# Kernel tuning notes

Hardware: AMD Instinct MI355X
Metric: run time of the kernel (lower is better)

## Reference

```python
import jax, jax.numpy as jnp
import numpy as np

N_NODES = 50000
N_EDGES = 800000
D = 128
N_GRAPHS = 64


def setup_inputs() -> dict:
    key = jax.random.key(0)
    ks = jax.random.split(key, 10)
    x = jax.random.normal(ks[0], (N_NODES, D), dtype=jnp.float32)
    edge_weight = jax.random.uniform(ks[1], (N_EDGES,), dtype=jnp.float32)
    W1 = jax.random.normal(ks[2], (D, D), dtype=jnp.float32) / np.sqrt(D)
    b1 = jax.random.normal(ks[3], (D,), dtype=jnp.float32) * 0.01
    W2 = jax.random.normal(ks[4], (D, D), dtype=jnp.float32) / np.sqrt(D)
    b2 = jax.random.normal(ks[5], (D,), dtype=jnp.float32) * 0.01
    Wh = jax.random.normal(ks[6], (D, 1), dtype=jnp.float32) / np.sqrt(D)
    bh = jax.random.normal(ks[7], (1,), dtype=jnp.float32) * 0.01
    edge_index = jax.random.randint(ks[8], (2, N_EDGES), 0, N_NODES, dtype=jnp.int64)
    batch = jnp.sort(jax.random.randint(ks[9], (N_NODES,), 0, N_GRAPHS, dtype=jnp.int64))
    return {"x": x, "edge_weight": edge_weight, "W1": W1, "b1": b1,
            "W2": W2, "b2": b2, "Wh": Wh, "bh": bh,
            "edge_index": edge_index, "batch": batch}


def reference(x, edge_weight, W1, b1, W2, b2, Wh, bh, edge_index, batch):
    N = x.shape[0]
    # --- GCN normalization with self-loops (computed once; shared by layers) ---
    row, col = edge_index[0], edge_index[1]
    loop = jnp.arange(N, dtype=edge_index.dtype)
    row2 = jnp.concatenate([row, loop])   # source nodes
    col2 = jnp.concatenate([col, loop])   # target nodes
    ew2 = jnp.concatenate([edge_weight, jnp.ones((N,), dtype=x.dtype)])
    deg = jax.ops.segment_sum(ew2, col2, num_segments=N)
    dinv = jnp.where(deg > 0, jax.lax.rsqrt(deg), 0.0)
    norm = dinv[row2] * ew2 * dinv[col2]  # [E+N]

    def gcn_conv(h, W, b):
        h = h @ W                                   # [N, D_out]
        msg = norm[:, None] * h[row2]               # gather + scale, [E+N, D_out]
        return jax.ops.segment_sum(msg, col2, num_segments=N) + b

    # dropout is identity in eval mode
    h = jax.nn.relu(gcn_conv(x, W1, b1))
    h = jax.nn.relu(gcn_conv(h, W2, b2))

    # --- global mean pool over graphs ---
    counts = jax.ops.segment_sum(jnp.ones((N,), dtype=h.dtype), batch, num_segments=N_GRAPHS)
    pooled = jax.ops.segment_sum(h, batch, num_segments=N_GRAPHS)
    pooled = pooled / jnp.maximum(counts, 1.0)[:, None]
    return pooled @ Wh + bh
```

## Files before the change

kernel.cpp:

```cpp
#include <hip/hip_runtime.h>
#include <hip/hip_bf16.h>
#include <hip/hip_fp16.h>
#include <hip/hip_fp8.h>

#define N_NODES  50000
#define N_EDGES  800000
#define D        128
#define N_GRAPHS 64
#define CAP      64
#define EW_SCALE 1048576.0f
#define NB_GEMM1 391
#define NB_FILL  3125
#define NB_AGG16 3125

typedef _Float16 half8 __attribute__((ext_vector_type(8)));
typedef float   float4v __attribute__((ext_vector_type(4)));
typedef float   f32x2   __attribute__((ext_vector_type(2)));

__device__ __forceinline__ float2 h2f(unsigned int u) {
    __half2 h = *reinterpret_cast<__half2*>(&u);
    return __half22float2(h);
}
__device__ __forceinline__ float hu2f(unsigned short u) {
    __half_raw hr; hr.x = u;
    return __half2float(__half(hr));
}
__device__ __forceinline__ float2 fp8x2_f32(unsigned short u) {
    f32x2 v = __builtin_amdgcn_cvt_pk_f32_fp8((int)u, false);
    return make_float2(v[0], v[1]);
}
__device__ __forceinline__ unsigned char f32_fp8(float f) {
    __hip_fp8_e4m3 q(f);
    return (unsigned char)q.__x;
}
__device__ __forceinline__ void unpack_pd(unsigned long long p, int& n, float& dv) {
    int c = (int)(p >> 40);
    n = c < CAP ? c : CAP;
    dv = rsqrtf(1.0f + (float)(p & 0xFFFFFFFFFFULL) * (1.0f / EW_SCALE));
}

__global__ __launch_bounds__(256) void fused_gemm1_fill(const float* __restrict__ X,
                                                        const float* __restrict__ W,
                                                        unsigned char* __restrict__ Y8,
                                                        const int* __restrict__ ei,
                                                        const float* __restrict__ ew,
                                                        unsigned long long* __restrict__ packed,
                                                        unsigned int* __restrict__ bucket) {
    __shared__ float XT[32 * 128];
    __shared__ float Ws[32 * 128];

    if (blockIdx.x >= NB_GEMM1) {
        int e = (blockIdx.x - NB_GEMM1) * 256 + threadIdx.x;
        if (e >= N_EDGES) return;
        int r = ei[e];
        int c = ei[N_EDGES + e];
        float w = ew[e];
        unsigned long long add = (1ULL << 40) | (unsigned long long)(unsigned)(w * EW_SCALE + 0.5f);
        unsigned long long old = atomicAdd(&packed[c], add);
        unsigned pos = (unsigned)(old >> 40);
        if (pos < CAP) {
            unsigned short wh = __half_as_ushort(__float2half_rn(w));
            bucket[(size_t)c * CAP + pos] = (unsigned)r | ((unsigned)wh << 16);
        }
        return;
    }

    const int tid  = threadIdx.x;
    const int row0 = blockIdx.x * 128;
    const int tr = tid >> 4, tc = tid & 15;
    float acc[8][8] = {};

    for (int kt = 0; kt < 4; kt++) {
        const int kbase = kt * 32;
        {
            const float4* src = (const float4*)(W + kbase * 128);
            float4* dst = (float4*)Ws;
            for (int i = tid; i < 1024; i += 256) dst[i] = src[i];
        }
        {
            int r  = tid >> 1;
            int rr = row0 + r; if (rr >= N_NODES) rr = N_NODES - 1;
            int k0 = (tid & 1) * 16;
            const float4* src = (const float4*)(X + (size_t)rr * 128 + kbase + k0);
#pragma unroll
            for (int i = 0; i < 4; i++) {
                float4 v = src[i];
                int k = k0 + i * 4;
                XT[(k + 0) * 128 + r] = v.x;
                XT[(k + 1) * 128 + r] = v.y;
                XT[(k + 2) * 128 + r] = v.z;
                XT[(k + 3) * 128 + r] = v.w;
            }
        }
        __syncthreads();
#pragma unroll 4
        for (int k = 0; k < 32; k++) {
            float xs[8], ws[8];
            *(float4*)&xs[0] = *(const float4*)(XT + k * 128 + tr * 8);
            *(float4*)&xs[4] = *(const float4*)(XT + k * 128 + tr * 8 + 4);
            *(float4*)&ws[0] = *(const float4*)(Ws + k * 128 + tc * 8);
            *(float4*)&ws[4] = *(const float4*)(Ws + k * 128 + tc * 8 + 4);
#pragma unroll
            for (int i = 0; i < 8; i++)
#pragma unroll
                for (int j = 0; j < 8; j++)
                    acc[i][j] += xs[i] * ws[j];
        }
        __syncthreads();
    }
#pragma unroll
    for (int i = 0; i < 8; i++) {
        int r = row0 + tr * 8 + i;
        if (r < N_NODES) {
            uint2 p;
            p.x = (unsigned)f32_fp8(acc[i][0]) | ((unsigned)f32_fp8(acc[i][1]) << 8)
                | ((unsigned)f32_fp8(acc[i][2]) << 16) | ((unsigned)f32_fp8(acc[i][3]) << 24);
            p.y = (unsigned)f32_fp8(acc[i][4]) | ((unsigned)f32_fp8(acc[i][5]) << 8)
                | ((unsigned)f32_fp8(acc[i][6]) << 16) | ((unsigned)f32_fp8(acc[i][7]) << 24);
            *(uint2*)(Y8 + (size_t)r * 128 + tc * 8) = p;
        }
    }
}

__global__ __launch_bounds__(512) void agg1_gemm2_kernel(const unsigned char* __restrict__ x8in,
                                                         const unsigned long long* __restrict__ packed,
                                                         const unsigned int* __restrict__ bucket,
                                                         const float* __restrict__ b1,
                                                         const float* __restrict__ W2,
                                                         unsigned char* __restrict__ x2) {
    __shared__ _Float16 sh1[16][136];
    const int wv   = threadIdx.x >> 6;
    const int lane = threadIdx.x & 63;
    const unsigned short* xs16 = (const unsigned short*)x8in;
    const int node0 = blockIdx.x * 16;

    float2 bb = ((const float2*)b1)[lane];

    const int nodeA = node0 + wv * 2;
    const int nodeB = nodeA + 1;
    int nA; float dvA; unpack_pd(packed[nodeA], nA, dvA);
    int nB; float dvB; unpack_pd(packed[nodeB], nB, dvB);

    unsigned pkA = 0u, pkB = 0u;
    if (lane < nA) {
        unsigned eh = bucket[(size_t)nodeA * CAP + lane];
        int src = eh & 0xFFFFu;
        int sn; float sdv; unpack_pd(packed[src], sn, sdv);
        float v = hu2f((unsigned short)(eh >> 16)) * sdv;
        pkA = (unsigned)src | ((unsigned)__half_as_ushort(__float2half_rn(v)) << 16);
    }
    if (lane < nB) {
        unsigned eh = bucket[(size_t)nodeB * CAP + lane];
        int src = eh & 0xFFFFu;
        int sn; float sdv; unpack_pd(packed[src], sn, sdv);
        float v = hu2f((unsigned short)(eh >> 16)) * sdv;
        pkB = (unsigned)src | ((unsigned)__half_as_ushort(__float2half_rn(v)) << 16);
    }
    int pkiA = (int)pkA, pkiB = (int)pkB;

    float2 xsA = fp8x2_f32(xs16[(size_t)nodeA * 64 + lane]);
    float2 xsB = fp8x2_f32(xs16[(size_t)nodeB * 64 + lane]);
    float aAx = dvA * xsA.x, aAy = dvA * xsA.y;
    float aBx = dvB * xsB.x, aBy = dvB * xsB.y;

    int nmax = nA > nB ? nA : nB;
    for (int i = 0; i < nmax; i += 4) {
        unsigned a0 = (unsigned)__shfl(pkiA, i);
        unsigned a1 = (unsigned)__shfl(pkiA, i + 1);
        unsigned a2 = (unsigned)__shfl(pkiA, i + 2);
        unsigned a3 = (unsigned)__shfl(pkiA, i + 3);
        unsigned b0 = (unsigned)__shfl(pkiB, i);
        unsigned b1u = (unsigned)__shfl(pkiB, i + 1);
        unsigned b2 = (unsigned)__shfl(pkiB, i + 2);
        unsigned b3 = (unsigned)__shfl(pkiB, i + 3);
        unsigned short mA0 = xs16[(size_t)(a0 & 0xFFFF) * 64 + lane];
        unsigned short mA1 = xs16[(size_t)(a1 & 0xFFFF) * 64 + lane];
        unsigned short mA2 = xs16[(size_t)(a2 & 0xFFFF) * 64 + lane];
        unsigned short mA3 = xs16[(size_t)(a3 & 0xFFFF) * 64 + lane];
        unsigned short mB0 = xs16[(size_t)(b0 & 0xFFFF) * 64 + lane];
        unsigned short mB1 = xs16[(size_t)(b1u & 0xFFFF) * 64 + lane];
        unsigned short mB2 = xs16[(size_t)(b2 & 0xFFFF) * 64 + lane];
        unsigned short mB3 = xs16[(size_t)(b3 & 0xFFFF) * 64 + lane];
        float2 fA0 = fp8x2_f32(mA0), fA1 = fp8x2_f32(mA1);
        float2 fA2 = fp8x2_f32(mA2), fA3 = fp8x2_f32(mA3);
        float2 fB0 = fp8x2_f32(mB0), fB1 = fp8x2_f32(mB1);
        float2 fB2 = fp8x2_f32(mB2), fB3 = fp8x2_f32(mB3);
        float vA0 = hu2f((unsigned short)(a0 >> 16));
        float vA1 = hu2f((unsigned short)(a1 >> 16));
        float vA2 = hu2f((unsigned short)(a2 >> 16));
        float vA3 = hu2f((unsigned short)(a3 >> 16));
        float vB0 = hu2f((unsigned short)(b0 >> 16));
        float vB1 = hu2f((unsigned short)(b1u >> 16));
        float vB2 = hu2f((unsigned short)(b2 >> 16));
        float vB3 = hu2f((unsigned short)(b3 >> 16));
        aAx += vA0*fA0.x + vA1*fA1.x + vA2*fA2.x + vA3*fA3.x;
        aAy += vA0*fA0.y + vA1*fA1.y + vA2*fA2.y + vA3*fA3.y;
        aBx += vB0*fB0.x + vB1*fB1.x + vB2*fB2.x + vB3*fB3.x;
        aBy += vB0*fB0.y + vB1*fB1.y + vB2*fB2.y + vB3*fB3.y;
    }

    float hAx = fmaxf(dvA * aAx + bb.x, 0.0f);
    float hAy = fmaxf(dvA * aAy + bb.y, 0.0f);
    float hBx = fmaxf(dvB * aBx + bb.x, 0.0f);
    float hBy = fmaxf(dvB * aBy + bb.y, 0.0f);
    sh1[wv * 2][lane * 2]         = (_Float16)hAx;
    sh1[wv * 2][lane * 2 + 1]     = (_Float16)hAy;
    sh1[wv * 2 + 1][lane * 2]     = (_Float16)hBx;
    sh1[wv * 2 + 1][lane * 2 + 1] = (_Float16)hBy;
    __syncthreads();

    const int quad = lane >> 4;
    const int l16  = lane & 15;
    float4v acc0 = {};
#pragma unroll
    for (int kc = 0; kc < 4; kc++) {
        const int k0 = kc * 32;
        half8 a = *(const half8*)(&sh1[l16][k0 + quad * 8]);
        const float* wp = W2 + (size_t)(k0 + quad * 8) * 128 + wv * 16 + l16;
        half8 b;
#pragma unroll
        for (int jj = 0; jj < 8; jj++) b[jj] = (_Float16)wp[jj * 128];
        acc0 = __builtin_amdgcn_mfma_f32_16x16x32_f16(a, b, acc0, 0, 0, 0);
    }
#pragma unroll
    for (int r = 0; r < 4; r++) {
        int row = node0 + quad * 4 + r;
        int rn; float s;
        unpack_pd(packed[row], rn, s);
        x2[(size_t)row * 128 + wv * 16 + l16] = f32_fp8(acc0[r] * s);
    }
}

__global__ __launch_bounds__(256) void agg_head_kernel(const unsigned char* __restrict__ x8,
                                                       const unsigned long long* __restrict__ packed,
                                                       const unsigned int* __restrict__ bucket,
                                                       const float* __restrict__ bias,
                                                       const float* __restrict__ Wh,
                                                       float* __restrict__ nodedot) {
    const int wv   = threadIdx.x >> 6;
    const int lane = threadIdx.x & 63;
    const unsigned short* xs16 = (const unsigned short*)x8;

    const int nodeA = blockIdx.x * 8 + wv * 2;
    const int nodeB = nodeA + 1;
    int nA; float dvA; unpack_pd(packed[nodeA], nA, dvA);
    int nB; float dvB; unpack_pd(packed[nodeB], nB, dvB);

    unsigned ehA = (lane < nA) ? bucket[(size_t)nodeA * CAP + lane] : 0u;
    unsigned ehB = (lane < nB) ? bucket[(size_t)nodeB * CAP + lane] : 0u;
    int eiA = (int)ehA, eiB = (int)ehB;

    float2 xsA = fp8x2_f32(xs16[(size_t)nodeA * 64 + lane]);
    float2 xsB = fp8x2_f32(xs16[(size_t)nodeB * 64 + lane]);
    float aAx = xsA.x, aAy = xsA.y;
    float aBx = xsB.x, aBy = xsB.y;

    int nmax = nA > nB ? nA : nB;
    for (int i = 0; i < nmax; i += 4) {
        unsigned a0 = (unsigned)__shfl(eiA, i);
        unsigned a1 = (unsigned)__shfl(eiA, i + 1);
        unsigned a2 = (unsigned)__shfl(eiA, i + 2);
        unsigned a3 = (unsigned)__shfl(eiA, i + 3);
        unsigned b0 = (unsigned)__shfl(eiB, i);
        unsigned b1u = (unsigned)__shfl(eiB, i + 1);
        unsigned b2 = (unsigned)__shfl(eiB, i + 2);
        unsigned b3 = (unsigned)__shfl(eiB, i + 3);
        unsigned short mA0 = xs16[(size_t)(a0 & 0xFFFF) * 64 + lane];
        unsigned short mA1 = xs16[(size_t)(a1 & 0xFFFF) * 64 + lane];
        unsigned short mA2 = xs16[(size_t)(a2 & 0xFFFF) * 64 + lane];
        unsigned short mA3 = xs16[(size_t)(a3 & 0xFFFF) * 64 + lane];
        unsigned short mB0 = xs16[(size_t)(b0 & 0xFFFF) * 64 + lane];
        unsigned short mB1 = xs16[(size_t)(b1u & 0xFFFF) * 64 + lane];
        unsigned short mB2 = xs16[(size_t)(b2 & 0xFFFF) * 64 + lane];
        unsigned short mB3 = xs16[(size_t)(b3 & 0xFFFF) * 64 + lane];
        float2 fA0 = fp8x2_f32(mA0), fA1 = fp8x2_f32(mA1);
        float2 fA2 = fp8x2_f32(mA2), fA3 = fp8x2_f32(mA3);
        float2 fB0 = fp8x2_f32(mB0), fB1 = fp8x2_f32(mB1);
        float2 fB2 = fp8x2_f32(mB2), fB3 = fp8x2_f32(mB3);
        float vA0 = hu2f((unsigned short)(a0 >> 16));
        float vA1 = hu2f((unsigned short)(a1 >> 16));
        float vA2 = hu2f((unsigned short)(a2 >> 16));
        float vA3 = hu2f((unsigned short)(a3 >> 16));
        float vB0 = hu2f((unsigned short)(b0 >> 16));
        float vB1 = hu2f((unsigned short)(b1u >> 16));
        float vB2 = hu2f((unsigned short)(b2 >> 16));
        float vB3 = hu2f((unsigned short)(b3 >> 16));
        aAx += vA0*fA0.x + vA1*fA1.x + vA2*fA2.x + vA3*fA3.x;
        aAy += vA0*fA0.y + vA1*fA1.y + vA2*fA2.y + vA3*fA3.y;
        aBx += vB0*fB0.x + vB1*fB1.x + vB2*fB2.x + vB3*fB3.x;
        aBy += vB0*fB0.y + vB1*fB1.y + vB2*fB2.y + vB3*fB3.y;
    }

    float2 b = ((const float2*)bias)[lane];
    float2 w = ((const float2*)Wh)[lane];
    float hAx = fmaxf(dvA * aAx + b.x, 0.0f);
    float hAy = fmaxf(dvA * aAy + b.y, 0.0f);
    float hBx = fmaxf(dvB * aBx + b.x, 0.0f);
    float hBy = fmaxf(dvB * aBy + b.y, 0.0f);
    float sA = hAx * w.x + hAy * w.y;
    float sB = hBx * w.x + hBy * w.y;
#pragma unroll
    for (int off = 32; off > 0; off >>= 1) {
        sA += __shfl_down(sA, off, 64);
        sB += __shfl_down(sB, off, 64);
    }
    if (lane == 0) {
        nodedot[nodeA] = sA;
        nodedot[nodeB] = sB;
    }
}

__global__ __launch_bounds__(256) void final2_kernel(const float* __restrict__ nodedot,
                                                     const int* __restrict__ batch,
                                                     const float* __restrict__ bh,
                                                     float* __restrict__ out) {
    __shared__ float red[256];
    int g = blockIdx.x;
    int lo = 0, hi = N_NODES;
    while (lo < hi) { int mid = (lo + hi) >> 1; if (batch[mid] < g) lo = mid + 1; else hi = mid; }
    int a = lo;
    hi = N_NODES;
    while (lo < hi) { int mid = (lo + hi) >> 1; if (batch[mid] < g + 1) lo = mid + 1; else hi = mid; }
    int b = lo;

    float s = 0.0f;
    for (int n = a + threadIdx.x; n < b; n += 256) s += nodedot[n];
    red[threadIdx.x] = s;
    __syncthreads();
#pragma unroll
    for (int off = 128; off > 0; off >>= 1) {
        if (threadIdx.x < off) red[threadIdx.x] += red[threadIdx.x + off];
        __syncthreads();
    }
    if (threadIdx.x == 0)
        out[g] = red[0] / fmaxf((float)(b - a), 1.0f) + bh[0];
}

extern "C" void kernel_launch(void* const* d_in, const int* in_sizes, int n_in,
                              void* d_out, int out_size, void* d_ws, size_t ws_size,
                              hipStream_t stream) {
    const float* x   = (const float*)d_in[0];
    const float* ew  = (const float*)d_in[1];
    const float* W1  = (const float*)d_in[2];
    const float* b1  = (const float*)d_in[3];
    const float* W2  = (const float*)d_in[4];
    const float* b2  = (const float*)d_in[5];
    const float* Wh  = (const float*)d_in[6];
    const float* bh  = (const float*)d_in[7];
    const int*   ei  = (const int*)d_in[8];
    const int*   bat = (const int*)d_in[9];
    float* out = (float*)d_out;

    char* ws = (char*)d_ws;
    unsigned char* bufA8 = (unsigned char*)ws;            ws += (size_t)N_NODES * D;
    unsigned char* bufB8 = (unsigned char*)ws;            ws += (size_t)N_NODES * D;
    ws += 128 - ((size_t)ws & 127);
    unsigned int* bucket = (unsigned int*)ws;             ws += (size_t)N_NODES * CAP * 4;
    unsigned long long* packed = (unsigned long long*)ws; ws += (size_t)N_NODES * 8;
    float*  nodedot = (float*)ws;                         ws += (size_t)N_NODES * 4;

    const int nb_agg8 = N_NODES / 8;

    hipMemsetAsync(packed, 0, (size_t)N_NODES * 8, stream);

    fused_gemm1_fill<<<NB_GEMM1 + NB_FILL, 256, 0, stream>>>(x, W1, bufA8, ei, ew, packed, bucket);

    agg1_gemm2_kernel<<<NB_AGG16, 512, 0, stream>>>(bufA8, packed, bucket, b1, W2, bufB8);

    agg_head_kernel<<<nb_agg8, 256, 0, stream>>>(bufB8, packed, bucket, b2, Wh, nodedot);

    final2_kernel<<<N_GRAPHS, 256, 0, stream>>>(nodedot, bat, bh, out);
}
```

Measured before the change: 205.4 us.

## Use fp16 MFMA for first GEMM and deepen gather unroll in aggregation

The first layer's X@W1 GEMM moves from a scalar FP32 outer-product loop to fp16 MFMA 16x16x32 instructions. X and a transposed W tile are staged in padded half-precision shared memory. Both aggregation kernels now gather eight neighbours per iteration instead of four, putting more loads in flight. The cost is fp16 rounding of inputs before the GEMM, byte-wise (uncoalesced-ish) fp8 output stores, and extra register pressure from the deeper unroll.

```diff
diff --git a/kernel.cpp b/kernel.cpp
--- a/kernel.cpp
+++ b/kernel.cpp
@@ -14,6 +14,7 @@
 #define NB_AGG16 3125
 
 typedef _Float16 half8 __attribute__((ext_vector_type(8)));
+typedef _Float16 half4 __attribute__((ext_vector_type(4)));
 typedef float   float4v __attribute__((ext_vector_type(4)));
 typedef float   f32x2   __attribute__((ext_vector_type(2)));
 
@@ -46,8 +47,8 @@
                                                         const float* __restrict__ ew,
                                                         unsigned long long* __restrict__ packed,
                                                         unsigned int* __restrict__ bucket) {
-    __shared__ float XT[32 * 128];
-    __shared__ float Ws[32 * 128];
+    __shared__ _Float16 Xs[128][72];
+    __shared__ _Float16 Wt[128][72];
 
     if (blockIdx.x >= NB_GEMM1) {
         int e = (blockIdx.x - NB_GEMM1) * 256 + threadIdx.x;
@@ -67,16 +68,15 @@
 
     const int tid  = threadIdx.x;
     const int row0 = blockIdx.x * 128;
-    const int tr = tid >> 4, tc = tid & 15;
-    float acc[8][8] = {};
+    const int wv   = tid >> 6;
+    const int lane = tid & 63;
+    const int quad = lane >> 4;
+    const int l16  = lane & 15;
+
+    float4v acc[8][2] = {};
 
     for (int kt = 0; kt < 4; kt++) {
         const int kbase = kt * 32;
-        {
-            const float4* src = (const float4*)(W + kbase * 128);
-            float4* dst = (float4*)Ws;
-            for (int i = tid; i < 1024; i += 256) dst[i] = src[i];
-        }
         {
             int r  = tid >> 1;
             int rr = row0 + r; if (rr >= N_NODES) rr = N_NODES - 1;
@@ -85,41 +85,47 @@
 #pragma unroll
             for (int i = 0; i < 4; i++) {
                 float4 v = src[i];
-                int k = k0 + i * 4;
-                XT[(k + 0) * 128 + r] = v.x;
-                XT[(k + 1) * 128 + r] = v.y;
-                XT[(k + 2) * 128 + r] = v.z;
-                XT[(k + 3) * 128 + r] = v.w;
+                half4 hv;
+                hv[0] = (_Float16)v.x; hv[1] = (_Float16)v.y;
+                hv[2] = (_Float16)v.z; hv[3] = (_Float16)v.w;
+                *(half4*)(&Xs[r][k0 + i * 4]) = hv;
             }
         }
+        {
+            int k  = tid >> 3;
+            int c0 = (tid & 7) * 16;
+            const float4* src = (const float4*)(W + (size_t)(kbase + k) * 128 + c0);
+#pragma unroll
+            for (int i = 0; i < 4; i++) {
+                float4 v = src[i];
+                Wt[c0 + i * 4 + 0][k] = (_Float16)v.x;
+                Wt[c0 + i * 4 + 1][k] = (_Float16)v.y;
+                Wt[c0 + i * 4 + 2][k] = (_Float16)v.z;
+                Wt[c0 + i * 4 + 3][k] = (_Float16)v.w;
+            }
+        }
         __syncthreads();
-#pragma unroll 4
-        for (int k = 0; k < 32; k++) {
-            float xs[8], ws[8];
-            *(float4*)&xs[0] = *(const float4*)(XT + k * 128 + tr * 8);
-            *(float4*)&xs[4] = *(const float4*)(XT + k * 128 + tr * 8 + 4);
-            *(float4*)&ws[0] = *(const float4*)(Ws + k * 128 + tc * 8);
-            *(float4*)&ws[4] = *(const float4*)(Ws + k * 128 + tc * 8 + 4);
-#pragma unroll
-            for (int i = 0; i < 8; i++)
-#pragma unroll
-                for (int j = 0; j < 8; j++)
-                    acc[i][j] += xs[i] * ws[j];
+
+        half8 b0 = *(const half8*)(&Wt[wv * 32 + l16][quad * 8]);
+        half8 b1f = *(const half8*)(&Wt[wv * 32 + 16 + l16][quad * 8]);
+#pragma unroll
+        for (int rt = 0; rt < 8; rt++) {
+            half8 a = *(const half8*)(&Xs[rt * 16 + l16][quad * 8]);
+            acc[rt][0] = __builtin_amdgcn_mfma_f32_16x16x32_f16(a, b0,  acc[rt][0], 0, 0, 0);
+            acc[rt][1] = __builtin_amdgcn_mfma_f32_16x16x32_f16(a, b1f, acc[rt][1], 0, 0, 0);
         }
         __syncthreads();
     }
 #pragma unroll
-    for (int i = 0; i < 8; i++) {
-        int r = row0 + tr * 8 + i;
-        if (r < N_NODES) {
-            uint2 p;
-            p.x = (unsigned)f32_fp8(acc[i][0]) | ((unsigned)f32_fp8(acc[i][1]) << 8)
-                | ((unsigned)f32_fp8(acc[i][2]) << 16) | ((unsigned)f32_fp8(acc[i][3]) << 24);
-            p.y = (unsigned)f32_fp8(acc[i][4]) | ((unsigned)f32_fp8(acc[i][5]) << 8)
-                | ((unsigned)f32_fp8(acc[i][6]) << 16) | ((unsigned)f32_fp8(acc[i][7]) << 24);
-            *(uint2*)(Y8 + (size_t)r * 128 + tc * 8) = p;
-        }
-    }
+    for (int rt = 0; rt < 8; rt++)
+#pragma unroll
+        for (int ct = 0; ct < 2; ct++)
+#pragma unroll
+            for (int r = 0; r < 4; r++) {
+                int row = row0 + rt * 16 + quad * 4 + r;
+                if (row < N_NODES)
+                    Y8[(size_t)row * 128 + wv * 32 + ct * 16 + l16] = f32_fp8(acc[rt][ct][r]);
+            }
 }
 
 __global__ __launch_bounds__(512) void agg1_gemm2_kernel(const unsigned char* __restrict__ x8in,
@@ -164,39 +170,30 @@
     float aBx = dvB * xsB.x, aBy = dvB * xsB.y;
 
     int nmax = nA > nB ? nA : nB;
-    for (int i = 0; i < nmax; i += 4) {
-        unsigned a0 = (unsigned)__shfl(pkiA, i);
-        unsigned a1 = (unsigned)__shfl(pkiA, i + 1);
-        unsigned a2 = (unsigned)__shfl(pkiA, i + 2);
-        unsigned a3 = (unsigned)__shfl(pkiA, i + 3);
-        unsigned b0 = (unsigned)__shfl(pkiB, i);
-        unsigned b1u = (unsigned)__shfl(pkiB, i + 1);
-        unsigned b2 = (unsigned)__shfl(pkiB, i + 2);
-        unsigned b3 = (unsigned)__shfl(pkiB, i + 3);
-        unsigned short mA0 = xs16[(size_t)(a0 & 0xFFFF) * 64 + lane];
-        unsigned short mA1 = xs16[(size_t)(a1 & 0xFFFF) * 64 + lane];
-        unsigned short mA2 = xs16[(size_t)(a2 & 0xFFFF) * 64 + lane];
-        unsigned short mA3 = xs16[(size_t)(a3 & 0xFFFF) * 64 + lane];
-        unsigned short mB0 = xs16[(size_t)(b0 & 0xFFFF) * 64 + lane];
-        unsigned short mB1 = xs16[(size_t)(b1u & 0xFFFF) * 64 + lane];
-        unsigned short mB2 = xs16[(size_t)(b2 & 0xFFFF) * 64 + lane];
-        unsigned short mB3 = xs16[(size_t)(b3 & 0xFFFF) * 64 + lane];
-        float2 fA0 = fp8x2_f32(mA0), fA1 = fp8x2_f32(mA1);
-        float2 fA2 = fp8x2_f32(mA2), fA3 = fp8x2_f32(mA3);
-        float2 fB0 = fp8x2_f32(mB0), fB1 = fp8x2_f32(mB1);
-        float2 fB2 = fp8x2_f32(mB2), fB3 = fp8x2_f32(mB3);
-        float vA0 = hu2f((unsigned short)(a0 >> 16));
-        float vA1 = hu2f((unsigned short)(a1 >> 16));
-        float vA2 = hu2f((unsigned short)(a2 >> 16));
-        float vA3 = hu2f((unsigned short)(a3 >> 16));
-        float vB0 = hu2f((unsigned short)(b0 >> 16));
-        float vB1 = hu2f((unsigned short)(b1u >> 16));
-        float vB2 = hu2f((unsigned short)(b2 >> 16));
-        float vB3 = hu2f((unsigned short)(b3 >> 16));
-        aAx += vA0*fA0.x + vA1*fA1.x + vA2*fA2.x + vA3*fA3.x;
-        aAy += vA0*fA0.y + vA1*fA1.y + vA2*fA2.y + vA3*fA3.y;
-        aBx += vB0*fB0.x + vB1*fB1.x + vB2*fB2.x + vB3*fB3.x;
-        aBy += vB0*fB0.y + vB1*fB1.y + vB2*fB2.y + vB3*fB3.y;
+    for (int i = 0; i < nmax; i += 8) {
+        unsigned av[8], bv[8];
+#pragma unroll
+        for (int j = 0; j < 8; j++) {
+            av[j] = (unsigned)__shfl(pkiA, i + j);
+            bv[j] = (unsigned)__shfl(pkiB, i + j);
+        }
+        unsigned short mA[8], mB[8];
+#pragma unroll
+        for (int j = 0; j < 8; j++) mA[j] = xs16[(size_t)(av[j] & 0xFFFFu) * 64 + lane];
+#pragma unroll
+        for (int j = 0; j < 8; j++) mB[j] = xs16[(size_t)(bv[j] & 0xFFFFu) * 64 + lane];
+#pragma unroll
+        for (int j = 0; j < 8; j++) {
+            float2 f = fp8x2_f32(mA[j]);
+            float v = hu2f((unsigned short)(av[j] >> 16));
+            aAx += v * f.x; aAy += v * f.y;
+        }
+#pragma unroll
+        for (int j = 0; j < 8; j++) {
+            float2 f = fp8x2_f32(mB[j]);
+            float v = hu2f((unsigned short)(bv[j] >> 16));
+            aBx += v * f.x; aBy += v * f.y;
+        }
     }
 
     float hAx = fmaxf(dvA * aAx + bb.x, 0.0f);
@@ -256,39 +253,30 @@
     float aBx = xsB.x, aBy = xsB.y;
 
     int nmax = nA > nB ? nA : nB;
-    for (int i = 0; i < nmax; i += 4) {
-        unsigned a0 = (unsigned)__shfl(eiA, i);
-        unsigned a1 = (unsigned)__shfl(eiA, i + 1);
-        unsigned a2 = (unsigned)__shfl(eiA, i + 2);
-        unsigned a3 = (unsigned)__shfl(eiA, i + 3);
-        unsigned b0 = (unsigned)__shfl(eiB, i);
-        unsigned b1u = (unsigned)__shfl(eiB, i + 1);
-        unsigned b2 = (unsigned)__shfl(eiB, i + 2);
-        unsigned b3 = (unsigned)__shfl(eiB, i + 3);
-        unsigned short mA0 = xs16[(size_t)(a0 & 0xFFFF) * 64 + lane];
-        unsigned short mA1 = xs16[(size_t)(a1 & 0xFFFF) * 64 + lane];
-        unsigned short mA2 = xs16[(size_t)(a2 & 0xFFFF) * 64 + lane];
-        unsigned short mA3 = xs16[(size_t)(a3 & 0xFFFF) * 64 + lane];
-        unsigned short mB0 = xs16[(size_t)(b0 & 0xFFFF) * 64 + lane];
-        unsigned short mB1 = xs16[(size_t)(b1u & 0xFFFF) * 64 + lane];
-        unsigned short mB2 = xs16[(size_t)(b2 & 0xFFFF) * 64 + lane];
-        unsigned short mB3 = xs16[(size_t)(b3 & 0xFFFF) * 64 + lane];
-        float2 fA0 = fp8x2_f32(mA0), fA1 = fp8x2_f32(mA1);
-        float2 fA2 = fp8x2_f32(mA2), fA3 = fp8x2_f32(mA3);
-        float2 fB0 = fp8x2_f32(mB0), fB1 = fp8x2_f32(mB1);
-        float2 fB2 = fp8x2_f32(mB2), fB3 = fp8x2_f32(mB3);
-        float vA0 = hu2f((unsigned short)(a0 >> 16));
-        float vA1 = hu2f((unsigned short)(a1 >> 16));
-        float vA2 = hu2f((unsigned short)(a2 >> 16));
-        float vA3 = hu2f((unsigned short)(a3 >> 16));
-        float vB0 = hu2f((unsigned short)(b0 >> 16));
-        float vB1 = hu2f((unsigned short)(b1u >> 16));
-        float vB2 = hu2f((unsigned short)(b2 >> 16));
-        float vB3 = hu2f((unsigned short)(b3 >> 16));
-        aAx += vA0*fA0.x + vA1*fA1.x + vA2*fA2.x + vA3*fA3.x;
-        aAy += vA0*fA0.y + vA1*fA1.y + vA2*fA2.y + vA3*fA3.y;
-        aBx += vB0*fB0.x + vB1*fB1.x + vB2*fB2.x + vB3*fB3.x;
-        aBy += vB0*fB0.y + vB1*fB1.y + vB2*fB2.y + vB3*fB3.y;
+    for (int i = 0; i < nmax; i += 8) {
+        unsigned av[8], bv[8];
+#pragma unroll
+        for (int j = 0; j < 8; j++) {
+            av[j] = (unsigned)__shfl(eiA, i + j);
+            bv[j] = (unsigned)__shfl(eiB, i + j);
+        }
+        unsigned short mA[8], mB[8];
+#pragma unroll
+        for (int j = 0; j < 8; j++) mA[j] = xs16[(size_t)(av[j] & 0xFFFFu) * 64 + lane];
+#pragma unroll
+        for (int j = 0; j < 8; j++) mB[j] = xs16[(size_t)(bv[j] & 0xFFFFu) * 64 + lane];
+#pragma unroll
+        for (int j = 0; j < 8; j++) {
+            float2 f = fp8x2_f32(mA[j]);
+            float v = hu2f((unsigned short)(av[j] >> 16));
+            aAx += v * f.x; aAy += v * f.y;
+        }
+#pragma unroll
+        for (int j = 0; j < 8; j++) {
+            float2 f = fp8x2_f32(mB[j]);
+            float v = hu2f((unsigned short)(bv[j] >> 16));
+            aBx += v * f.x; aBy += v * f.y;
+        }
     }
 
     float2 b = ((const float2*)bias)[lane];
```

New measurement: 198.8 us. -3.2%, faster.
